# Optimization experiments

Hardware: AMD Instinct MI355X
Metric: run time of the kernel (lower is better)

The kernel has to match this reference:

```python
import jax, jax.numpy as jnp
import numpy as np

T = 3        # temporal_aggregation_size
DH = 32      # cfg.dim_head
EPS = 1e-6   # cfg.norm_eps


def _ln(x, w, b):
    mu = jnp.mean(x, axis=-1, keepdims=True)
    var = jnp.mean(jnp.square(x - mu), axis=-1, keepdims=True)
    return (x - mu) * jax.lax.rsqrt(var + EPS) * w + b


def setup_inputs() -> dict:
    key = jax.random.key(0)
    ks = jax.random.split(key, 8)
    B, H, W, C = 48, 56, 56, 256
    hid = 4 * C
    s = 0.02
    return {
        "x": jax.random.normal(ks[0], (B, H, W, C), jnp.float32),
        "norm1_w": jnp.ones((C,), jnp.float32),
        "norm1_b": jnp.zeros((C,), jnp.float32),
        "kvq_w": jax.random.normal(ks[1], (3 * C, C), jnp.float32) * s,
        "kvq_b": jnp.zeros((3 * C,), jnp.float32),
        "proj_w": jax.random.normal(ks[2], (C, C), jnp.float32) * s,
        "proj_b": jnp.zeros((C,), jnp.float32),
        "norm2_w": jnp.ones((C,), jnp.float32),
        "norm2_b": jnp.zeros((C,), jnp.float32),
        "fc1_w": jax.random.normal(ks[3], (hid, C), jnp.float32) * s,
        "fc1_b": jnp.zeros((hid,), jnp.float32),
        "fc2_w": jax.random.normal(ks[4], (C, hid), jnp.float32) * s,
        "fc2_b": jnp.zeros((C,), jnp.float32),
    }


def reference(x, norm1_w, norm1_b, kvq_w, kvq_b, proj_w, proj_b,
              norm2_w, norm2_b, fc1_w, fc1_b, fc2_w, fc2_b):
    B, H, W, C = x.shape
    nh = C // DH
    scale = DH ** -0.5

    # [B,H,W,C] -> [(B/T)*H*W, T, C]: group frames of the same clip together per pixel
    def to_tokens(y):
        return y.reshape(B // T, T, H, W, C).transpose(0, 2, 3, 1, 4).reshape(-1, T, C)

    xn = to_tokens(_ln(x, norm1_w, norm1_b))           # [N, T, C]
    N = xn.shape[0]

    kvq = xn @ kvq_w.T + kvq_b                          # [N, T, 3C]
    kvq = kvq.reshape(N, T, 3, nh, DH).transpose(0, 3, 2, 1, 4)  # [N, nh, 3, T, DH]
    k, v, q = kvq[:, :, 0], kvq[:, :, 1], kvq[:, :, 2]  # kvq order per source unbind

    attn = jax.nn.softmax(jnp.einsum('nhqd,nhkd->nhqk', q, k) * scale, axis=-1)
    out = jnp.einsum('nhqk,nhkd->nhqd', attn, v)        # [N, nh, T, DH]
    out = out.transpose(0, 2, 1, 3).reshape(N, T, C)
    out = out @ proj_w.T + proj_b

    xt = out + to_tokens(x)                             # residual in token layout

    h = _ln(xt, norm2_w, norm2_b)
    h = jax.nn.gelu(h @ fc1_w.T + fc1_b, approximate=False)
    xt = xt + (h @ fc2_w.T + fc2_b)

    # back to [B,H,W,C]
    return xt.reshape(B // T, H, W, T, C).transpose(0, 3, 1, 2, 4).reshape(B, H, W, C)
```

## Files before the change

### kernel.cpp

```cpp
#include <hip/hip_runtime.h>
#include <cstdint>
#include <cstddef>

typedef unsigned short u16;
typedef unsigned int u32;
typedef __attribute__((ext_vector_type(4))) float f32x4;
typedef __attribute__((ext_vector_type(8))) short s16x8;

#define DEVI static __device__ __forceinline__

DEVI float bf2f(u16 v) { return __uint_as_float(((u32)v) << 16); }
DEVI u16 f2bf(float f) {
  u32 u = __float_as_uint(f);
  u = u + 0x7fffu + ((u >> 16) & 1u);
  return (u16)(u >> 16);
}
DEVI float gelu_f(float x) {
  float u = 0.7978845608028654f * (x + 0.044715f * x * x * x);
  float e = __expf(2.0f * u);
  float t = 1.0f - 2.0f / (e + 1.0f);
  return 0.5f * x * (1.0f + t);
}
DEVI void gload_lds16(const void* g, void* l) {
  __builtin_amdgcn_global_load_lds(
      (const __attribute__((address_space(1))) u32*)g,
      (__attribute__((address_space(3))) u32*)l, 16, 0, 0);
}

template<int IN_BF16>
__global__ __launch_bounds__(256) void ln_kernel(
    const void* __restrict__ inv, const float* __restrict__ w,
    const float* __restrict__ b, u16* __restrict__ out, int nrows)
{
  const int wid = (blockIdx.x << 2) + (threadIdx.x >> 6);
  const int lane = threadIdx.x & 63;
  if (wid >= nrows) return;
  float v[4];
  if (IN_BF16) {
    const ushort4 raw = *((const ushort4*)inv + (size_t)wid * 64 + lane);
    v[0] = bf2f(raw.x); v[1] = bf2f(raw.y); v[2] = bf2f(raw.z); v[3] = bf2f(raw.w);
  } else {
    const float4 raw = *((const float4*)inv + (size_t)wid * 64 + lane);
    v[0] = raw.x; v[1] = raw.y; v[2] = raw.z; v[3] = raw.w;
  }
  float s = v[0] + v[1] + v[2] + v[3];
  #pragma unroll
  for (int m = 1; m < 64; m <<= 1) s += __shfl_xor(s, m, 64);
  const float mu = s * (1.0f / 256.0f);
  const float d0 = v[0] - mu, d1 = v[1] - mu, d2 = v[2] - mu, d3 = v[3] - mu;
  float q = d0 * d0 + d1 * d1 + d2 * d2 + d3 * d3;
  #pragma unroll
  for (int m = 1; m < 64; m <<= 1) q += __shfl_xor(q, m, 64);
  const float rstd = rsqrtf(q * (1.0f / 256.0f) + 1e-6f);
  const int c = lane << 2;
  ushort4 o;
  o.x = f2bf(d0 * rstd * w[c + 0] + b[c + 0]);
  o.y = f2bf(d1 * rstd * w[c + 1] + b[c + 1]);
  o.z = f2bf(d2 * rstd * w[c + 2] + b[c + 2]);
  o.w = f2bf(d3 * rstd * w[c + 3] + b[c + 3]);
  *((ushort4*)out + (size_t)wid * 64 + lane) = o;
}

__global__ __launch_bounds__(256) void cvt_kernel(
    const float* __restrict__ in, u16* __restrict__ out, int n)
{
  const int i = blockIdx.x * 256 + threadIdx.x;
  if (i < n) out[i] = f2bf(in[i]);
}

template<int EPI>
__global__ __launch_bounds__(256) void gemm_bt(
    const u16* __restrict__ A, const u16* __restrict__ Bw,
    const float* __restrict__ bias, const void* __restrict__ res,
    void* __restrict__ Cout, int M, int N, int K)
{
  __shared__ u16 lds[16384];
  const int tid = threadIdx.x;
  const int lane = tid & 63;
  const int wave = tid >> 6;
  const int wr = wave >> 1;
  const int wc = wave & 1;
  const int mtile = blockIdx.y;
  const int ntile = blockIdx.x;

  const u16* Abase = A + (size_t)mtile * 128 * K;
  const u16* Bbase = Bw + (size_t)ntile * 128 * K;

  f32x4 acc[4][4] = {};

  const int nk = K >> 6;
  for (int kt = 0; kt < nk; ++kt) {
    const int k0 = kt << 6;
    #pragma unroll
    for (int i = 0; i < 4; ++i) {
      const int L = i * 256 + tid;
      const int r = L >> 3;
      const int c = (L & 7) ^ (r & 7);
      gload_lds16(Abase + (size_t)r * K + k0 + c * 8,
                  &lds[(i * 256 + (wave << 6)) * 8]);
    }
    #pragma unroll
    for (int i = 0; i < 4; ++i) {
      const int L = i * 256 + tid;
      const int r = L >> 3;
      const int c = (L & 7) ^ (r & 7);
      gload_lds16(Bbase + (size_t)r * K + k0 + c * 8,
                  &lds[8192 + (i * 256 + (wave << 6)) * 8]);
    }
    __syncthreads();
    #pragma unroll
    for (int kk = 0; kk < 2; ++kk) {
      s16x8 af[4], bfv[4];
      #pragma unroll
      for (int i = 0; i < 4; ++i) {
        const int row = (wr << 6) + (i << 4) + (lane & 15);
        const int cc = ((kk << 2) + (lane >> 4)) ^ (row & 7);
        af[i] = *(const s16x8*)&lds[row * 64 + cc * 8];
      }
      #pragma unroll
      for (int j = 0; j < 4; ++j) {
        const int row = (wc << 6) + (j << 4) + (lane & 15);
        const int cc = ((kk << 2) + (lane >> 4)) ^ (row & 7);
        bfv[j] = *(const s16x8*)&lds[8192 + row * 64 + cc * 8];
      }
      #pragma unroll
      for (int i = 0; i < 4; ++i)
        #pragma unroll
        for (int j = 0; j < 4; ++j)
          acc[i][j] = __builtin_amdgcn_mfma_f32_16x16x32_bf16(af[i], bfv[j], acc[i][j], 0, 0, 0);
    }
    __syncthreads();
  }

  #pragma unroll
  for (int j = 0; j < 4; ++j) {
    const int col = (ntile << 7) + (wc << 6) + (j << 4) + (lane & 15);
    const float bv = bias[col];
    #pragma unroll
    for (int i = 0; i < 4; ++i) {
      const int rbase = (mtile << 7) + (wr << 6) + (i << 4) + ((lane >> 4) << 2);
      #pragma unroll
      for (int p = 0; p < 4; ++p) {
        const size_t off = (size_t)(rbase + p) * N + col;
        float v = acc[i][j][p] + bv;
        if (EPI == 0) {
          ((u16*)Cout)[off] = f2bf(v);
        } else if (EPI == 1) {
          ((u16*)Cout)[off] = f2bf(gelu_f(v));
        } else if (EPI == 2) {
          v += ((const float*)res)[off];
          ((u16*)Cout)[off] = f2bf(v);
        } else {
          v += bf2f(((const u16*)res)[off]);
          ((float*)Cout)[off] = v;
        }
      }
    }
  }
}

DEVI void load32bf(float* dst, const u16* p) {
  #pragma unroll
  for (int i = 0; i < 4; ++i) {
    const uint4 r = *(const uint4*)(p + i * 8);
    const u32 w0 = r.x, w1 = r.y, w2 = r.z, w3 = r.w;
    dst[i*8+0] = bf2f((u16)(w0 & 0xffffu)); dst[i*8+1] = bf2f((u16)(w0 >> 16));
    dst[i*8+2] = bf2f((u16)(w1 & 0xffffu)); dst[i*8+3] = bf2f((u16)(w1 >> 16));
    dst[i*8+4] = bf2f((u16)(w2 & 0xffffu)); dst[i*8+5] = bf2f((u16)(w2 >> 16));
    dst[i*8+6] = bf2f((u16)(w3 & 0xffffu)); dst[i*8+7] = bf2f((u16)(w3 >> 16));
  }
}

__global__ __launch_bounds__(256) void attn_kernel(
    const u16* __restrict__ kvq, u16* __restrict__ aout, int nrows)
{
  const int t = blockIdx.x * 256 + threadIdx.x;
  if (t >= nrows * 8) return;
  const int lr = t >> 3;
  const int h = t & 7;
  const int gl = lr / 9408;
  const int rem = lr - gl * 9408;
  const int hw = rem % 3136;
  const int base = gl * 9408 + hw;

  float q[32];
  load32bf(q, kvq + (size_t)lr * 768 + 512 + h * 32);

  float l[3];
  #pragma unroll
  for (int tk = 0; tk < 3; ++tk) {
    float kv[32];
    load32bf(kv, kvq + (size_t)(base + tk * 3136) * 768 + h * 32);
    float a = 0.f;
    #pragma unroll
    for (int i = 0; i < 32; ++i) a += q[i] * kv[i];
    l[tk] = a * 0.17677669529663687f;
  }
  const float m = fmaxf(l[0], fmaxf(l[1], l[2]));
  const float e0 = __expf(l[0] - m), e1 = __expf(l[1] - m), e2 = __expf(l[2] - m);
  const float inv = 1.0f / (e0 + e1 + e2);
  const float ew[3] = {e0 * inv, e1 * inv, e2 * inv};

  float o[32] = {};
  #pragma unroll
  for (int tk = 0; tk < 3; ++tk) {
    float kv[32];
    load32bf(kv, kvq + (size_t)(base + tk * 3136) * 768 + 256 + h * 32);
    #pragma unroll
    for (int i = 0; i < 32; ++i) o[i] += ew[tk] * kv[i];
  }
  u16* op = aout + (size_t)lr * 256 + h * 32;
  #pragma unroll
  for (int i = 0; i < 4; ++i) {
    uint4 r;
    r.x = (u32)f2bf(o[i*8+0]) | ((u32)f2bf(o[i*8+1]) << 16);
    r.y = (u32)f2bf(o[i*8+2]) | ((u32)f2bf(o[i*8+3]) << 16);
    r.z = (u32)f2bf(o[i*8+4]) | ((u32)f2bf(o[i*8+5]) << 16);
    r.w = (u32)f2bf(o[i*8+6]) | ((u32)f2bf(o[i*8+7]) << 16);
    *(uint4*)(op + i * 8) = r;
  }
}

extern "C" void kernel_launch(void* const* d_in, const int* in_sizes, int n_in,
                              void* d_out, int out_size, void* d_ws, size_t ws_size,
                              hipStream_t stream) {
  const float* x    = (const float*)d_in[0];
  const float* n1w  = (const float*)d_in[1];
  const float* n1b  = (const float*)d_in[2];
  const float* kvqw = (const float*)d_in[3];
  const float* kvqb = (const float*)d_in[4];
  const float* pw   = (const float*)d_in[5];
  const float* pb   = (const float*)d_in[6];
  const float* n2w  = (const float*)d_in[7];
  const float* n2b  = (const float*)d_in[8];
  const float* f1w  = (const float*)d_in[9];
  const float* f1b  = (const float*)d_in[10];
  const float* f2w  = (const float*)d_in[11];
  const float* f2b  = (const float*)d_in[12];

  char* ws = (char*)d_ws;
  u16* xn     = (u16*)(ws + 0);
  u16* aout   = (u16*)(ws + 77070336);
  u16* kvqc   = (u16*)(ws + 154140672);
  u16* hbuf   = kvqc;
  u16* xt     = xn;
  u16* xn2    = aout;
  u16* wbuf   = (u16*)(ws + 231211008);
  u16* kvqw_b = wbuf;
  u16* pw_b   = wbuf + 196608;
  u16* f1w_b  = wbuf + 262144;
  u16* f2w_b  = wbuf + 524288;

  cvt_kernel<<<768,  256, 0, stream>>>(kvqw, kvqw_b, 196608);
  cvt_kernel<<<256,  256, 0, stream>>>(pw,   pw_b,   65536);
  cvt_kernel<<<1024, 256, 0, stream>>>(f1w,  f1w_b,  262144);
  cvt_kernel<<<1024, 256, 0, stream>>>(f2w,  f2w_b,  262144);

  ln_kernel<0><<<37632, 256, 0, stream>>>(x, n1w, n1b, xn, 150528);

  for (int c = 0; c < 4; ++c) {
    const size_t r0 = (size_t)c * 37632;
    gemm_bt<0><<<dim3(6, 294), 256, 0, stream>>>(
        xn + r0 * 256, kvqw_b, kvqb, nullptr, kvqc, 37632, 768, 256);
    attn_kernel<<<1176, 256, 0, stream>>>(kvqc, aout + r0 * 256, 37632);
  }

  gemm_bt<2><<<dim3(2, 1176), 256, 0, stream>>>(
      aout, pw_b, pb, x, xt, 150528, 256, 256);

  ln_kernel<1><<<37632, 256, 0, stream>>>(xt, n2w, n2b, xn2, 150528);

  for (int c = 0; c < 4; ++c) {
    const size_t r0 = (size_t)c * 37632;
    gemm_bt<1><<<dim3(8, 294), 256, 0, stream>>>(
        xn2 + r0 * 256, f1w_b, f1b, nullptr, hbuf, 37632, 1024, 256);
    gemm_bt<3><<<dim3(2, 294), 256, 0, stream>>>(
        hbuf, f2w_b, f2b, xt + r0 * 256, (float*)d_out + r0 * 256, 37632, 256, 1024);
  }
}
```

Measured before the change: 1.088 ms.

## Use 256x256 GEMM tiles with double-buffered LDS prefetch

```diff
diff --git a/kernel.cpp b/kernel.cpp
--- a/kernel.cpp
+++ b/kernel.cpp
@@ -25,6 +25,11 @@
   __builtin_amdgcn_global_load_lds(
       (const __attribute__((address_space(1))) u32*)g,
       (__attribute__((address_space(3))) u32*)l, 16, 0, 0);
+}
+DEVI void wait_vm0_bar() {
+  asm volatile("s_waitcnt vmcnt(0)" ::: "memory");
+  __builtin_amdgcn_s_barrier();
+  asm volatile("" ::: "memory");
 }
 
 template<int IN_BF16>
@@ -69,80 +74,95 @@
 }
 
 template<int EPI>
-__global__ __launch_bounds__(256) void gemm_bt(
+__global__ __launch_bounds__(512, 2) void gemm2(
     const u16* __restrict__ A, const u16* __restrict__ Bw,
     const float* __restrict__ bias, const void* __restrict__ res,
     void* __restrict__ Cout, int M, int N, int K)
 {
-  __shared__ u16 lds[16384];
+  extern __shared__ u16 lds[];
   const int tid = threadIdx.x;
   const int lane = tid & 63;
   const int wave = tid >> 6;
-  const int wr = wave >> 1;
-  const int wc = wave & 1;
+  const int wr = wave >> 2;
+  const int wn = wave & 3;
   const int mtile = blockIdx.y;
   const int ntile = blockIdx.x;
 
-  const u16* Abase = A + (size_t)mtile * 128 * K;
-  const u16* Bbase = Bw + (size_t)ntile * 128 * K;
-
-  f32x4 acc[4][4] = {};
-
+  const u16* Abase = A + (size_t)mtile * 256 * K;
+  const u16* Bbase = Bw + (size_t)ntile * 256 * K;
+
+  f32x4 acc[8][4] = {};
   const int nk = K >> 6;
-  for (int kt = 0; kt < nk; ++kt) {
+
+  auto STAGE = [&](int b, int kt) {
     const int k0 = kt << 6;
+    const int bb = b << 15;
     #pragma unroll
     for (int i = 0; i < 4; ++i) {
-      const int L = i * 256 + tid;
+      const int L = (i << 9) + tid;
       const int r = L >> 3;
       const int c = (L & 7) ^ (r & 7);
-      gload_lds16(Abase + (size_t)r * K + k0 + c * 8,
-                  &lds[(i * 256 + (wave << 6)) * 8]);
+      gload_lds16(Abase + (size_t)r * K + k0 + (c << 3),
+                  &lds[bb + (((i << 9) + (wave << 6)) << 3)]);
     }
     #pragma unroll
     for (int i = 0; i < 4; ++i) {
-      const int L = i * 256 + tid;
+      const int L = (i << 9) + tid;
       const int r = L >> 3;
       const int c = (L & 7) ^ (r & 7);
-      gload_lds16(Bbase + (size_t)r * K + k0 + c * 8,
-                  &lds[8192 + (i * 256 + (wave << 6)) * 8]);
+      gload_lds16(Bbase + (size_t)r * K + k0 + (c << 3),
+                  &lds[bb + 16384 + (((i << 9) + (wave << 6)) << 3)]);
     }
-    __syncthreads();
+  };
+
+  auto COMPUTE = [&](int b) {
+    const u16* La = &lds[b << 15];
+    const u16* Lb = &lds[(b << 15) + 16384];
     #pragma unroll
     for (int kk = 0; kk < 2; ++kk) {
-      s16x8 af[4], bfv[4];
+      s16x8 af[8], bfv[4];
       #pragma unroll
-      for (int i = 0; i < 4; ++i) {
-        const int row = (wr << 6) + (i << 4) + (lane & 15);
+      for (int m = 0; m < 8; ++m) {
+        const int row = (wr << 7) + (m << 4) + (lane & 15);
         const int cc = ((kk << 2) + (lane >> 4)) ^ (row & 7);
-        af[i] = *(const s16x8*)&lds[row * 64 + cc * 8];
+        af[m] = *(const s16x8*)&La[(row << 6) + (cc << 3)];
       }
       #pragma unroll
-      for (int j = 0; j < 4; ++j) {
-        const int row = (wc << 6) + (j << 4) + (lane & 15);
+      for (int n = 0; n < 4; ++n) {
+        const int row = (wn << 6) + (n << 4) + (lane & 15);
         const int cc = ((kk << 2) + (lane >> 4)) ^ (row & 7);
-        bfv[j] = *(const s16x8*)&lds[8192 + row * 64 + cc * 8];
+        bfv[n] = *(const s16x8*)&Lb[(row << 6) + (cc << 3)];
       }
       #pragma unroll
-      for (int i = 0; i < 4; ++i)
+      for (int m = 0; m < 8; ++m)
         #pragma unroll
-        for (int j = 0; j < 4; ++j)
-          acc[i][j] = __builtin_amdgcn_mfma_f32_16x16x32_bf16(af[i], bfv[j], acc[i][j], 0, 0, 0);
+        for (int n = 0; n < 4; ++n)
+          acc[m][n] = __builtin_amdgcn_mfma_f32_16x16x32_bf16(af[m], bfv[n], acc[m][n], 0, 0, 0);
     }
-    __syncthreads();
-  }
-
-  #pragma unroll
-  for (int j = 0; j < 4; ++j) {
-    const int col = (ntile << 7) + (wc << 6) + (j << 4) + (lane & 15);
+  };
+
+  STAGE(0, 0);
+  wait_vm0_bar();
+  int cur = 0;
+  for (int kt = 0; kt < nk - 1; ++kt) {
+    STAGE(cur ^ 1, kt + 1);
+    COMPUTE(cur);
+    wait_vm0_bar();
+    cur ^= 1;
+  }
+  COMPUTE(cur);
+
+  #pragma unroll
+  for (int n = 0; n < 4; ++n) {
+    const int col = (ntile << 8) + (wn << 6) + (n << 4) + (lane & 15);
     const float bv = bias[col];
     #pragma unroll
-    for (int i = 0; i < 4; ++i) {
-      const int rbase = (mtile << 7) + (wr << 6) + (i << 4) + ((lane >> 4) << 2);
+    for (int m = 0; m < 8; ++m) {
+      const int rbase = (mtile << 8) + (wr << 7) + (m << 4) + ((lane >> 4) << 2);
       #pragma unroll
       for (int p = 0; p < 4; ++p) {
         const size_t off = (size_t)(rbase + p) * N + col;
-        float v = acc[i][j][p] + bv;
+        float v = acc[m][n][p] + bv;
         if (EPI == 0) {
           ((u16*)Cout)[off] = f2bf(v);
         } else if (EPI == 1) {
@@ -260,21 +280,21 @@
 
   for (int c = 0; c < 4; ++c) {
     const size_t r0 = (size_t)c * 37632;
-    gemm_bt<0><<<dim3(6, 294), 256, 0, stream>>>(
+    gemm2<0><<<dim3(3, 147), 512, 131072, stream>>>(
         xn + r0 * 256, kvqw_b, kvqb, nullptr, kvqc, 37632, 768, 256);
     attn_kernel<<<1176, 256, 0, stream>>>(kvqc, aout + r0 * 256, 37632);
   }
 
-  gemm_bt<2><<<dim3(2, 1176), 256, 0, stream>>>(
+  gemm2<2><<<dim3(1, 588), 512, 131072, stream>>>(
       aout, pw_b, pb, x, xt, 150528, 256, 256);
 
   ln_kernel<1><<<37632, 256, 0, stream>>>(xt, n2w, n2b, xn2, 150528);
 
   for (int c = 0; c < 4; ++c) {
     const size_t r0 = (size_t)c * 37632;
-    gemm_bt<1><<<dim3(8, 294), 256, 0, stream>>>(
+    gemm2<1><<<dim3(4, 147), 512, 131072, stream>>>(
         xn2 + r0 * 256, f1w_b, f1b, nullptr, hbuf, 37632, 1024, 256);
-    gemm_bt<3><<<dim3(2, 294), 256, 0, stream>>>(
+    gemm2<3><<<dim3(1, 147), 512, 131072, stream>>>(
         hbuf, f2w_b, f2b, xt + r0 * 256, (float*)d_out + r0 * 256, 37632, 256, 1024);
   }
 }
```

Result: slower. 1.256 ms (+15.4%).
